# Optimization experiments

Hardware: AMD Instinct MI355X
Metric: run time of the kernel (lower is better)

## Reference

```python
import jax, jax.numpy as jnp
import numpy as np

B, LQ, LK = 4, 2048, 2048
XS, YS, PD = 1024, 1024, 128


def setup_inputs() -> dict:
    key = jax.random.key(0)
    ks = jax.random.split(key, 8)
    s_x = 1.0 / np.sqrt(XS)
    s_y = 1.0 / np.sqrt(YS)
    return {
        "x": jax.random.normal(ks[0], (B, LQ, XS), dtype=jnp.float32),
        "y": jax.random.normal(ks[1], (B, LK, YS), dtype=jnp.float32),
        "Wq": jax.random.normal(ks[2], (XS, PD), dtype=jnp.float32) * s_x,
        "bq": jax.random.normal(ks[3], (PD,), dtype=jnp.float32) * 0.01,
        "Wk": jax.random.normal(ks[4], (YS, PD), dtype=jnp.float32) * s_y,
        "bk": jax.random.normal(ks[5], (PD,), dtype=jnp.float32) * 0.01,
        "Wv": jax.random.normal(ks[6], (YS, PD), dtype=jnp.float32) * s_y,
        "bv": jax.random.normal(ks[7], (PD,), dtype=jnp.float32) * 0.01,
        "mask": 1,
    }


def reference(x, y, Wq, bq, Wk, bk, Wv, bv, mask):
    # Projections (torch Linear: x @ W^T + b; here weights stored as [in, out])
    q = x @ Wq + bq  # [B, LQ, PD]
    k = y @ Wk + bk  # [B, LK, PD]
    v = y @ Wv + bv  # [B, LK, PD]
    scale = 1.0 / jnp.sqrt(jnp.asarray(PD, dtype=q.dtype))
    att = jax.nn.softmax(jnp.einsum("bqd,bkd->bqk", q, k) * scale, axis=-1)
    if mask:
        # NOTE: faithful to original — triu applied AFTER softmax (diagonal=1),
        # zeroing the lower triangle + diagonal without renormalizing.
        att = jnp.triu(att, k=1)
    return jnp.einsum("bqk,bkd->bqd", att, v)  # [B, LQ, PD]
```

## Files before the change

### kernel.cpp

```cpp
#include <hip/hip_runtime.h>

typedef short s8v __attribute__((ext_vector_type(8)));
typedef float f4v __attribute__((ext_vector_type(4)));

#define NB 4
#define LQ 2048
#define LKK 2048
#define XS 1024
#define PDD 128

#define PST 68
#define AST 132

__device__ __forceinline__ ushort f2bf(float x) {
  union { float f; uint u; } v; v.f = x;
  uint r = (v.u + 0x7fffu + ((v.u >> 16) & 1u)) >> 16;
  return (ushort)r;
}

__global__ __launch_bounds__(256) void k_wtrans(const float* __restrict__ Wq,
                                                const float* __restrict__ Wk,
                                                const float* __restrict__ Wv,
                                                ushort* __restrict__ Wt) {
  int p = blockIdx.y;
  const float* W = (p == 0) ? Wq : (p == 1) ? Wk : Wv;
  ushort* out = Wt + (size_t)p * (PDD * XS);
  int t = threadIdx.x;
  int n = t >> 1;
  int kk0 = (t & 1) * 16;
  int k0 = blockIdx.x * 32;
  ushort tmp[16];
#pragma unroll
  for (int i = 0; i < 16; ++i) tmp[i] = f2bf(W[(size_t)(k0 + kk0 + i) * PDD + n]);
  uint4 u0, u1;
  u0.x = tmp[0] | ((uint)tmp[1] << 16);  u0.y = tmp[2] | ((uint)tmp[3] << 16);
  u0.z = tmp[4] | ((uint)tmp[5] << 16);  u0.w = tmp[6] | ((uint)tmp[7] << 16);
  u1.x = tmp[8] | ((uint)tmp[9] << 16);  u1.y = tmp[10] | ((uint)tmp[11] << 16);
  u1.z = tmp[12] | ((uint)tmp[13] << 16); u1.w = tmp[14] | ((uint)tmp[15] << 16);
  uint4* dst = (uint4*)&out[n * XS + k0 + kk0];
  dst[0] = u0; dst[1] = u1;
}

__global__ __launch_bounds__(256, 3) void k_proj(const float* __restrict__ x,
                                                 const float* __restrict__ y,
                                                 const ushort* __restrict__ Wt,
                                                 const float* __restrict__ bq,
                                                 const float* __restrict__ bk,
                                                 const float* __restrict__ bv,
                                                 ushort* __restrict__ qo,
                                                 ushort* __restrict__ ko,
                                                 ushort* __restrict__ vt) {
  int bx = blockIdx.x;
  int p = bx >> 8;
  int tile = bx & 255;
  const float* in = (p == 0) ? x : y;
  const ushort* wt = Wt + (size_t)p * (PDD * XS);
  int row0 = tile * 32;
  __shared__ ushort As[32 * 72];
  __shared__ ushort Bs[128 * 72];
  int t = threadIdx.x, wave = t >> 6, lane = t & 63, quad = lane >> 4, lc = lane & 15;

  int ar = t >> 3, ac0 = (t & 7) * 8;
  int bn = t >> 1, bk0 = (t & 1) * 32;
  const float* asrc = in + (size_t)(row0 + ar) * XS + ac0;
  const ushort* bsrc = wt + (size_t)bn * XS + bk0;

  float4 ra0, ra1;
  uint4 rb0, rb1, rb2, rb3;
  auto load = [&](int k0) {
    const float* ap = asrc + k0;
    ra0 = *(const float4*)ap;
    ra1 = *(const float4*)(ap + 4);
    const ushort* bp = bsrc + k0;
    rb0 = *(const uint4*)bp;
    rb1 = *(const uint4*)(bp + 8);
    rb2 = *(const uint4*)(bp + 16);
    rb3 = *(const uint4*)(bp + 24);
  };
  auto store = [&]() {
    uint4 pa;
    pa.x = f2bf(ra0.x) | ((uint)f2bf(ra0.y) << 16);
    pa.y = f2bf(ra0.z) | ((uint)f2bf(ra0.w) << 16);
    pa.z = f2bf(ra1.x) | ((uint)f2bf(ra1.y) << 16);
    pa.w = f2bf(ra1.z) | ((uint)f2bf(ra1.w) << 16);
    *(uint4*)&As[ar * 72 + ac0] = pa;
    *(uint4*)&Bs[bn * 72 + bk0] = rb0;
    *(uint4*)&Bs[bn * 72 + bk0 + 8] = rb1;
    *(uint4*)&Bs[bn * 72 + bk0 + 16] = rb2;
    *(uint4*)&Bs[bn * 72 + bk0 + 24] = rb3;
  };

  const f4v z4 = {0.f, 0.f, 0.f, 0.f};
  f4v acc[2][2];
#pragma unroll
  for (int m = 0; m < 2; ++m)
#pragma unroll
    for (int n = 0; n < 2; ++n) acc[m][n] = z4;

  load(0);
#pragma unroll 1
  for (int k0 = 0; k0 < XS; k0 += 64) {
    store();
    __syncthreads();
    load((k0 + 64) & (XS - 1));
#pragma unroll
    for (int kc = 0; kc < 2; ++kc) {
      s8v a0 = *(const s8v*)&As[lc * 72 + kc * 32 + quad * 8];
      s8v a1 = *(const s8v*)&As[(16 + lc) * 72 + kc * 32 + quad * 8];
      s8v b0 = *(const s8v*)&Bs[(wave * 32 + lc) * 72 + kc * 32 + quad * 8];
      s8v b1 = *(const s8v*)&Bs[(wave * 32 + 16 + lc) * 72 + kc * 32 + quad * 8];
      acc[0][0] = __builtin_amdgcn_mfma_f32_16x16x32_bf16(a0, b0, acc[0][0], 0, 0, 0);
      acc[0][1] = __builtin_amdgcn_mfma_f32_16x16x32_bf16(a0, b1, acc[0][1], 0, 0, 0);
      acc[1][0] = __builtin_amdgcn_mfma_f32_16x16x32_bf16(a1, b0, acc[1][0], 0, 0, 0);
      acc[1][1] = __builtin_amdgcn_mfma_f32_16x16x32_bf16(a1, b1, acc[1][1], 0, 0, 0);
    }
    __syncthreads();
  }

  const float qscale = 0.08838834764831845f;
  const float* bias = (p == 0) ? bq : (p == 1) ? bk : bv;
  if (p < 2) {
    ushort* o = (p == 0) ? qo : ko;
    float scl = (p == 0) ? qscale : 1.0f;
#pragma unroll
    for (int m = 0; m < 2; ++m)
#pragma unroll
      for (int n = 0; n < 2; ++n) {
        int col = wave * 32 + n * 16 + lc;
        float bb = bias[col];
#pragma unroll
        for (int g = 0; g < 4; ++g) {
          int r = row0 + m * 16 + quad * 4 + g;
          o[(size_t)r * PDD + col] = f2bf((acc[m][n][g] + bb) * scl);
        }
      }
  } else {
#pragma unroll
    for (int m = 0; m < 2; ++m) {
      int rbase = row0 + m * 16 + quad * 4;
      int b = rbase >> 11, rr = rbase & 2047;
#pragma unroll
      for (int n = 0; n < 2; ++n) {
        int col = wave * 32 + n * 16 + lc;
        float bb = bias[col];
        ushort4 pk;
        pk.x = f2bf(acc[m][n][0] + bb);
        pk.y = f2bf(acc[m][n][1] + bb);
        pk.z = f2bf(acc[m][n][2] + bb);
        pk.w = f2bf(acc[m][n][3] + bb);
        *(ushort4*)&vt[((size_t)(b * PDD + col)) * LKK + rr] = pk;
      }
    }
  }
}

__global__ __launch_bounds__(512, 2) void k_attn(const ushort* __restrict__ qg,
                                                 const ushort* __restrict__ kg,
                                                 const ushort* __restrict__ vtg,
                                                 const int* __restrict__ maskp,
                                                 float* __restrict__ out) {
  __shared__ float smem[8 * 32 * PST];
  __shared__ float lS[8][2][16];
  int bx = blockIdx.x;
  int xcd = bx & 7;
  int b = xcd >> 1;
  int q0 = ((bx >> 3) * 2 + (xcd & 1)) * 32;
  int t = threadIdx.x;
  int wave = t >> 6, lane = t & 63, quad = lane >> 4, lc = lane & 15;
  int domask = *maskp;
  float* Psw = smem + wave * (32 * PST);

  s8v aq[2][4];
#pragma unroll
  for (int m = 0; m < 2; ++m) {
    const ushort* qrow = qg + ((size_t)(b * LQ + q0 + m * 16 + lc)) * PDD + quad * 8;
#pragma unroll
    for (int kc = 0; kc < 4; ++kc) aq[m][kc] = *(const s8v*)(qrow + kc * 32);
  }

  const f4v z4 = {0.f, 0.f, 0.f, 0.f};
  f4v acc[2][8];
#pragma unroll
  for (int m = 0; m < 2; ++m)
#pragma unroll
    for (int i = 0; i < 8; ++i) acc[m][i] = z4;
  float rs[2][4] = {{0.f, 0.f, 0.f, 0.f}, {0.f, 0.f, 0.f, 0.f}};

  const ushort* kbase = kg + ((size_t)(b * LKK + wave * 64 + lc)) * PDD + quad * 8;
  const ushort* vbase = vtg + ((size_t)(b * PDD + lc)) * LKK + wave * 64 + quad * 8;

#pragma unroll 1
  for (int i = 0; i < 4; ++i) {
    int kt = wave + i * 8;
    const ushort* kp = kbase + (size_t)(i * 512) * PDD;

    s8v kf[16];
#pragma unroll
    for (int nt = 0; nt < 4; ++nt)
#pragma unroll
      for (int kc = 0; kc < 4; ++kc)
        kf[nt * 4 + kc] = *(const s8v*)(kp + (size_t)(nt * 16) * PDD + kc * 32);

    f4v sf[2][4];
#pragma unroll
    for (int nt = 0; nt < 4; ++nt) {
      f4v s0 = z4, s1 = z4;
#pragma unroll
      for (int kc = 0; kc < 4; ++kc) {
        s0 = __builtin_amdgcn_mfma_f32_16x16x32_bf16(aq[0][kc], kf[nt * 4 + kc], s0, 0, 0, 0);
        s1 = __builtin_amdgcn_mfma_f32_16x16x32_bf16(aq[1][kc], kf[nt * 4 + kc], s1, 0, 0, 0);
      }
      sf[0][nt] = s0;
      sf[1][nt] = s1;
    }

    s8v vf[16];
#pragma unroll
    for (int dt = 0; dt < 8; ++dt) {
      vf[dt]     = *(const s8v*)(vbase + (size_t)(dt * 16) * LKK + i * 512);
      vf[8 + dt] = *(const s8v*)(vbase + (size_t)(dt * 16) * LKK + i * 512 + 32);
    }
    __builtin_amdgcn_sched_barrier(0);

#pragma unroll
    for (int m = 0; m < 2; ++m)
#pragma unroll
      for (int g = 0; g < 4; ++g) {
        int rg = q0 + m * 16 + quad * 4 + g;
#pragma unroll
        for (int nt = 0; nt < 4; ++nt) {
          float pv = __expf(sf[m][nt][g]);
          rs[m][g] += pv;
          int jg = kt * 64 + nt * 16 + lc;
          if (domask && (jg <= rg)) pv = 0.f;
          Psw[(m * 16 + quad * 4 + g) * PST + nt * 16 + lc] = pv;
        }
      }

#pragma unroll
    for (int jc = 0; jc < 2; ++jc)
#pragma unroll
      for (int m = 0; m < 2; ++m) {
        const float* pp = &Psw[(m * 16 + lc) * PST + jc * 32 + quad * 8];
        float4 p0 = *(const float4*)pp;
        float4 p1 = *(const float4*)(pp + 4);
        s8v ap;
        ap[0] = (short)f2bf(p0.x); ap[1] = (short)f2bf(p0.y);
        ap[2] = (short)f2bf(p0.z); ap[3] = (short)f2bf(p0.w);
        ap[4] = (short)f2bf(p1.x); ap[5] = (short)f2bf(p1.y);
        ap[6] = (short)f2bf(p1.z); ap[7] = (short)f2bf(p1.w);
#pragma unroll
        for (int dt = 0; dt < 8; ++dt) {
          acc[m][dt] = __builtin_amdgcn_mfma_f32_16x16x32_bf16(ap, vf[jc * 8 + dt], acc[m][dt], 0, 0, 0);
        }
      }
  }

#pragma unroll
  for (int off = 8; off >= 1; off >>= 1)
#pragma unroll
    for (int m = 0; m < 2; ++m)
#pragma unroll
      for (int g = 0; g < 4; ++g) rs[m][g] += __shfl_xor(rs[m][g], off, 64);

  __syncthreads();
  if (lc == 0) {
#pragma unroll
    for (int m = 0; m < 2; ++m)
#pragma unroll
      for (int g = 0; g < 4; ++g) lS[wave][m][quad * 4 + g] = rs[m][g];
  }

#pragma unroll
  for (int m = 0; m < 2; ++m) {
#pragma unroll
    for (int dt = 0; dt < 8; ++dt)
#pragma unroll
      for (int g = 0; g < 4; ++g)
        smem[wave * (16 * AST) + (quad * 4 + g) * AST + dt * 16 + lc] = acc[m][dt][g];
    __syncthreads();
    {
      int row = t >> 5, c0 = (t & 31) * 4;
      float L = 0.f;
      float ox = 0.f, oy = 0.f, oz = 0.f, ow = 0.f;
#pragma unroll
      for (int p = 0; p < 8; ++p) {
        L += lS[p][m][row];
        const float* a = &smem[p * (16 * AST) + row * AST + c0];
        float4 xv = *(const float4*)a;
        ox += xv.x; oy += xv.y; oz += xv.z; ow += xv.w;
      }
      float inv = 1.0f / L;
      float4 o;
      o.x = ox * inv; o.y = oy * inv; o.z = oz * inv; o.w = ow * inv;
      float* op = out + ((size_t)(b * LQ + q0 + m * 16 + row)) * PDD + c0;
      *(float4*)op = o;
    }
    __syncthreads();
  }
}

extern "C" void kernel_launch(void* const* d_in, const int* in_sizes, int n_in,
                              void* d_out, int out_size, void* d_ws, size_t ws_size,
                              hipStream_t stream) {
  const float* x  = (const float*)d_in[0];
  const float* y  = (const float*)d_in[1];
  const float* Wq = (const float*)d_in[2];
  const float* bq = (const float*)d_in[3];
  const float* Wk = (const float*)d_in[4];
  const float* bk = (const float*)d_in[5];
  const float* Wv = (const float*)d_in[6];
  const float* bv = (const float*)d_in[7];
  const int* mask = (const int*)d_in[8];
  char* ws = (char*)d_ws;
  ushort* qb = (ushort*)(ws);
  ushort* kb = (ushort*)(ws + (size_t)(1 << 21));
  ushort* vt = (ushort*)(ws + (size_t)(2 << 21));
  ushort* Wt = (ushort*)(ws + (size_t)(3 << 21));
  float* out = (float*)d_out;

  hipLaunchKernelGGL(k_wtrans, dim3(32, 3), dim3(256), 0, stream, Wq, Wk, Wv, Wt);
  hipLaunchKernelGGL(k_proj, dim3(768), dim3(256), 0, stream, x, y, Wt, bq, bk, bv, qb, kb, vt);
  hipLaunchKernelGGL(k_attn, dim3(256), dim3(512), 0, stream, qb, kb, vt, mask, out);
}
```

Before: 160.6 us.

## Store Q/K/V in MFMA fragment-packed layout for coalesced attention loads

The projection kernel now writes Q, K and transposed V in a layout pre-swizzled to the MFMA operand fragments, so each lane's 8-element vector sits contiguously at lane*8 within a 512-element block. The attention kernel then loads Q, K and V fragments with fully contiguous per-wave 1 KB reads instead of strided row accesses. This is meant to cut global-memory transaction count and cache-line waste in the attention loop. In exchange, the projection epilogue uses scattered, less coalesced stores and the two kernels become tightly coupled to the packed format.

```diff
diff --git a/kernel.cpp b/kernel.cpp
--- a/kernel.cpp
+++ b/kernel.cpp
@@ -17,6 +17,7 @@
   uint r = (v.u + 0x7fffu + ((v.u >> 16) & 1u)) >> 16;
   return (ushort)r;
 }
+
 
 __global__ __launch_bounds__(256) void k_wtrans(const float* __restrict__ Wq,
                                                 const float* __restrict__ Wk,
@@ -122,33 +123,40 @@
   if (p < 2) {
     ushort* o = (p == 0) ? qo : ko;
     float scl = (p == 0) ? qscale : 1.0f;
-#pragma unroll
-    for (int m = 0; m < 2; ++m)
+    int bb2 = row0 >> 11;
+    int rloc = row0 & 2047;
+#pragma unroll
+    for (int m = 0; m < 2; ++m) {
+      int qt = (rloc >> 4) + m;
 #pragma unroll
       for (int n = 0; n < 2; ++n) {
         int col = wave * 32 + n * 16 + lc;
         float bb = bias[col];
-#pragma unroll
-        for (int g = 0; g < 4; ++g) {
-          int r = row0 + m * 16 + quad * 4 + g;
-          o[(size_t)r * PDD + col] = f2bf((acc[m][n][g] + bb) * scl);
-        }
-      }
+        size_t base = ((((size_t)(bb2 * 128 + qt) * 4 + wave) * 4 + (n * 2 + (lc >> 3))) * 16 +
+                       quad * 4) * 8 + (lc & 7);
+#pragma unroll
+        for (int g = 0; g < 4; ++g)
+          o[base + (size_t)g * 8] = f2bf((acc[m][n][g] + bb) * scl);
+      }
+    }
   } else {
 #pragma unroll
     for (int m = 0; m < 2; ++m) {
       int rbase = row0 + m * 16 + quad * 4;
-      int b = rbase >> 11, rr = rbase & 2047;
+      int bb2 = rbase >> 11, rr = rbase & 2047;
+      int kchunk = rr >> 5, qv = (rr >> 3) & 3, jj0 = rr & 7;
 #pragma unroll
       for (int n = 0; n < 2; ++n) {
         int col = wave * 32 + n * 16 + lc;
+        int dt = wave * 2 + n;
         float bb = bias[col];
         ushort4 pk;
         pk.x = f2bf(acc[m][n][0] + bb);
         pk.y = f2bf(acc[m][n][1] + bb);
         pk.z = f2bf(acc[m][n][2] + bb);
         pk.w = f2bf(acc[m][n][3] + bb);
-        *(ushort4*)&vt[((size_t)(b * PDD + col)) * LKK + rr] = pk;
+        size_t off = ((((size_t)(bb2 * 64 + kchunk) * 8 + dt) * 4 + qv) * 16 + lc) * 8 + jj0;
+        *(ushort4*)&vt[off] = pk;
       }
     }
   }
@@ -170,13 +178,13 @@
   int domask = *maskp;
   float* Psw = smem + wave * (32 * PST);
 
+  const ushort* qB = qg + ((size_t)(b * 128 + (q0 >> 4))) * 2048 + lane * 8;
   s8v aq[2][4];
 #pragma unroll
-  for (int m = 0; m < 2; ++m) {
-    const ushort* qrow = qg + ((size_t)(b * LQ + q0 + m * 16 + lc)) * PDD + quad * 8;
-#pragma unroll
-    for (int kc = 0; kc < 4; ++kc) aq[m][kc] = *(const s8v*)(qrow + kc * 32);
-  }
+  for (int m = 0; m < 2; ++m)
+#pragma unroll
+    for (int kc = 0; kc < 4; ++kc)
+      aq[m][kc] = *(const s8v*)(qB + m * 2048 + kc * 512);
 
   const f4v z4 = {0.f, 0.f, 0.f, 0.f};
   f4v acc[2][8];
@@ -185,21 +193,15 @@
 #pragma unroll
     for (int i = 0; i < 8; ++i) acc[m][i] = z4;
   float rs[2][4] = {{0.f, 0.f, 0.f, 0.f}, {0.f, 0.f, 0.f, 0.f}};
-
-  const ushort* kbase = kg + ((size_t)(b * LKK + wave * 64 + lc)) * PDD + quad * 8;
-  const ushort* vbase = vtg + ((size_t)(b * PDD + lc)) * LKK + wave * 64 + quad * 8;
 
 #pragma unroll 1
   for (int i = 0; i < 4; ++i) {
     int kt = wave + i * 8;
-    const ushort* kp = kbase + (size_t)(i * 512) * PDD;
-
+
+    const ushort* kB = kg + ((size_t)(b * 128 + i * 32 + wave * 4)) * 2048 + lane * 8;
     s8v kf[16];
 #pragma unroll
-    for (int nt = 0; nt < 4; ++nt)
-#pragma unroll
-      for (int kc = 0; kc < 4; ++kc)
-        kf[nt * 4 + kc] = *(const s8v*)(kp + (size_t)(nt * 16) * PDD + kc * 32);
+    for (int f = 0; f < 16; ++f) kf[f] = *(const s8v*)(kB + f * 512);
 
     f4v sf[2][4];
 #pragma unroll
@@ -214,12 +216,10 @@
       sf[1][nt] = s1;
     }
 
+    const ushort* vB = vtg + ((size_t)(b * 64 + i * 16 + wave * 2)) * 4096 + lane * 8;
     s8v vf[16];
 #pragma unroll
-    for (int dt = 0; dt < 8; ++dt) {
-      vf[dt]     = *(const s8v*)(vbase + (size_t)(dt * 16) * LKK + i * 512);
-      vf[8 + dt] = *(const s8v*)(vbase + (size_t)(dt * 16) * LKK + i * 512 + 32);
-    }
+    for (int f = 0; f < 16; ++f) vf[f] = *(const s8v*)(vB + f * 512);
     __builtin_amdgcn_sched_barrier(0);
 
 #pragma unroll
```

Measured after the change: 142.1 us. 1.13x faster.
